# Kernel tuning notes

Measured on AMD Instinct MI355X. Metric: run time of the kernel, lower is better.

Reference implementation:

```python
import jax, jax.numpy as jnp
import numpy as np
from jax import lax

B, T, F = 64, 1536, 512
POOL = 6
UNITS = 256
NUM_CLASSES = 250


def _hard_sigmoid(x):
    # Keras hard_sigmoid: clip(0.2*x + 0.5, 0, 1)
    return jnp.clip(0.2 * x + 0.5, 0.0, 1.0)


def setup_inputs() -> dict:
    key = jax.random.key(0)
    ks = jax.random.split(key, 6)
    x = jax.random.normal(ks[0], (B, T, F), dtype=jnp.float32)
    # ConvLSTM1D with kernel_size=1 over a length-1 spatial axis == dense gates.
    W = jax.random.normal(ks[1], (F, 4 * UNITS), dtype=jnp.float32) * 0.05   # input kernel
    R = jax.random.normal(ks[2], (UNITS, 4 * UNITS), dtype=jnp.float32) * 0.05  # recurrent kernel
    b = jnp.zeros((4 * UNITS,), dtype=jnp.float32)
    Wd = jax.random.normal(ks[3], (UNITS, NUM_CLASSES), dtype=jnp.float32) * 0.05
    bd = jnp.zeros((NUM_CLASSES,), dtype=jnp.float32)
    return {"x": x, "W": W, "R": R, "b": b, "Wd": Wd, "bd": bd}


def reference(x, W, R, b, Wd, bd):
    Bx, Tx, Fx = x.shape
    Tp = Tx // POOL
    # AveragePooling1D(pool_size=6) over time
    xp = x[:, : Tp * POOL].reshape(Bx, Tp, POOL, Fx).mean(axis=2)  # [B, Tp, F]
    # Precompute input-to-gate contribution for all steps (one big GEMM)
    zx = jnp.einsum('btf,fg->btg', xp, W) + b  # [B, Tp, 4U]
    z_seq = jnp.swapaxes(zx, 0, 1)  # [Tp, B, 4U]

    h0 = jnp.zeros((Bx, UNITS), dtype=x.dtype)
    c0 = jnp.zeros((Bx, UNITS), dtype=x.dtype)

    def step(carry, z_t):
        h, c = carry
        z = z_t + h @ R  # [B, 4U]
        i, f, g, o = jnp.split(z, 4, axis=-1)  # Keras gate order: i, f, c, o
        i = _hard_sigmoid(i)
        f = _hard_sigmoid(f)
        g = jnp.tanh(g)
        o = _hard_sigmoid(o)
        c = f * c + i * g
        h = o * jnp.tanh(c)
        return (h, c), None

    (h, _), _ = lax.scan(step, (h0, c0), z_seq)
    # squeeze(-2) + dropout(eval: identity) + flatten -> [B, UNITS]
    logits = h @ Wd + bd
    return jax.nn.softmax(logits, axis=-1)
```

## Files before the change

### kernel.cpp

```cpp
#include <hip/hip_runtime.h>
#include <hip/hip_bf16.h>

#define BB 64
#define TT 1536
#define FF 512
#define TP 256
#define UU 256
#define GG 1024
#define NC 250

typedef _Float16 h2_t __attribute__((ext_vector_type(2)));
typedef _Float16 f16x8 __attribute__((ext_vector_type(8)));
typedef float f32x4 __attribute__((ext_vector_type(4)));

#if defined(__has_builtin)
#  if __has_builtin(__builtin_amdgcn_fdot2)
#    define FDOT2(a, b, c) __builtin_amdgcn_fdot2((a), (b), (c), false)
#  endif
#endif
#ifndef FDOT2
__device__ __forceinline__ float fdot2_fb(h2_t a, h2_t b, float c) {
    return c + (float)a[0] * (float)b[0] + (float)a[1] * (float)b[1];
}
#  define FDOT2(a, b, c) fdot2_fb((a), (b), (c))
#endif

#define BC(u) __builtin_bit_cast(h2_t, (u))

__device__ __forceinline__ float hsig(float z) {
    return fminf(fmaxf(fmaf(z, 0.2f, 0.5f), 0.0f), 1.0f);
}

__device__ __forceinline__ float ftanh(float x) {
    float ax = fabsf(x);
    float e = __expf(-2.0f * ax);
    float t = (1.0f - e) / (1.0f + e);
    return copysignf(t, x);
}

__device__ __forceinline__ void dot4(float& z, const uint4& r, const uint4& h) {
    z = FDOT2(BC(r.x), BC(h.x), z);
    z = FDOT2(BC(r.y), BC(h.y), z);
    z = FDOT2(BC(r.z), BC(h.z), z);
    z = FDOT2(BC(r.w), BC(h.w), z);
}

#if defined(__has_builtin) && __has_builtin(__builtin_amdgcn_mov_dpp)
template <int CTRL>
__device__ __forceinline__ float qperm(float v) {
    return __builtin_bit_cast(float,
        __builtin_amdgcn_mov_dpp(__builtin_bit_cast(int, v), CTRL, 0xf, 0xf, true));
}
#else
template <int CTRL>
__device__ __forceinline__ float qperm(float v) {
    return __shfl_xor(v, CTRL == 0xB1 ? 1 : 2, 64);
}
#endif

__global__ __launch_bounds__(256) void pool_kernel(const float* __restrict__ x,
                                                   _Float16* __restrict__ xph) {
    int idx = blockIdx.x * 256 + threadIdx.x;
    int f4 = (idx & 127) << 2;
    int m = idx >> 7;
    int tp = m & (TP - 1);
    int b = m >> 8;
    const float* src = x + ((size_t)b * TT + (size_t)tp * 6) * FF + f4;
    float sx = 0.f, sy = 0.f, sz = 0.f, sw = 0.f;
#pragma unroll
    for (int j = 0; j < 6; ++j) {
        float4 v = *(const float4*)&src[j * FF];
        sx += v.x; sy += v.y; sz += v.z; sw += v.w;
    }
    const float r6 = 1.0f / 6.0f;
    h2_t lo, hi;
    lo[0] = (_Float16)(sx * r6); lo[1] = (_Float16)(sy * r6);
    hi[0] = (_Float16)(sz * r6); hi[1] = (_Float16)(sw * r6);
    float2 w = make_float2(__builtin_bit_cast(float, lo), __builtin_bit_cast(float, hi));
    *(float2*)&xph[(size_t)m * FF + f4] = w;
}

template <int PERM>
__global__ __launch_bounds__(256) void transpose_cvt(const float* __restrict__ in,
                                                     _Float16* __restrict__ out,
                                                     int K, int N) {
    __shared__ _Float16 tile[32][42];
    const int r = threadIdx.x >> 3;
    const int c4 = (threadIdx.x & 7) << 2;
    const int n0 = blockIdx.x << 5;
    const int k0 = blockIdx.y << 5;
    float4 v = *(const float4*)&in[(size_t)(k0 + r) * N + n0 + c4];
    tile[r][c4 + 0] = (_Float16)v.x;
    tile[r][c4 + 1] = (_Float16)v.y;
    tile[r][c4 + 2] = (_Float16)v.z;
    tile[r][c4 + 3] = (_Float16)v.w;
    __syncthreads();
    int n = n0 + r;
    int orow = PERM ? (((n & 255) << 2) | (n >> 8)) : n;
    h2_t lo, hi;
    lo[0] = tile[c4 + 0][r]; lo[1] = tile[c4 + 1][r];
    hi[0] = tile[c4 + 2][r]; hi[1] = tile[c4 + 3][r];
    float2 w = make_float2(__builtin_bit_cast(float, lo), __builtin_bit_cast(float, hi));
    *(float2*)&out[(size_t)orow * K + k0 + c4] = w;
}

__global__ __launch_bounds__(256, 2) void gemm_zx_mfma(const _Float16* __restrict__ Ah,
                                                       const _Float16* __restrict__ Bt,
                                                       const float* __restrict__ bias,
                                                       float* __restrict__ C) {
    __shared__ _Float16 As[128 * 40];
    __shared__ _Float16 Bs[128 * 40];
    const int tid = threadIdx.x;
    const int bn = blockIdx.x * 128;
    const int bm = blockIdx.y * 128;
    const int wave = tid >> 6, lane = tid & 63;
    const int wm = (wave & 1) * 64, wn = (wave >> 1) * 64;
    const int l15 = lane & 15, q8 = (lane >> 4) * 8;
    const int srow = tid >> 1, shalf = tid & 1;

    f32x4 acc[4][4] = {};
    const uint4* ag = (const uint4*)(Ah + (size_t)(bm + srow) * FF);
    const uint4* bg = (const uint4*)(Bt + (size_t)(bn + srow) * FF);
    uint4* as_st = (uint4*)As + 5 * srow + 2 * shalf;
    uint4* bs_st = (uint4*)Bs + 5 * srow + 2 * shalf;

    for (int k0 = 0; k0 < FF; k0 += 32) {
        int qi = (k0 >> 3) + shalf * 2;
        uint4 a0 = ag[qi], a1 = ag[qi + 1];
        uint4 b0 = bg[qi], b1 = bg[qi + 1];
        __syncthreads();
        as_st[0] = a0; as_st[1] = a1;
        bs_st[0] = b0; bs_st[1] = b1;
        __syncthreads();
        f16x8 af[4], bf[4];
#pragma unroll
        for (int mt = 0; mt < 4; ++mt)
            af[mt] = *(const f16x8*)&As[(wm + 16 * mt + l15) * 40 + q8];
#pragma unroll
        for (int nt = 0; nt < 4; ++nt)
            bf[nt] = *(const f16x8*)&Bs[(wn + 16 * nt + l15) * 40 + q8];
#pragma unroll
        for (int mt = 0; mt < 4; ++mt)
#pragma unroll
            for (int nt = 0; nt < 4; ++nt)
                acc[mt][nt] = __builtin_amdgcn_mfma_f32_16x16x32_f16(af[mt], bf[nt],
                                                                    acc[mt][nt], 0, 0, 0);
    }
    const int rq = (lane >> 4) * 4;
#pragma unroll
    for (int nt = 0; nt < 4; ++nt) {
        int col = bn + wn + 16 * nt + l15;
        int oc = ((col & 3) << 8) | (col >> 2);
        float bv = bias[oc];
#pragma unroll
        for (int mt = 0; mt < 4; ++mt) {
#pragma unroll
            for (int r = 0; r < 4; ++r) {
                int row = bm + wm + 16 * mt + rq + r;
                C[(size_t)row * GG + col] = ((const float*)&acc[mt][nt])[r] + bv;
            }
        }
    }
}

__global__ __launch_bounds__(512, 1) void lstm_scan(const float* __restrict__ zx,
                                                    const _Float16* __restrict__ Rt,
                                                    float* __restrict__ hfin) {
    __shared__ uint4 Rl[14][512];
    __shared__ __align__(16) _Float16 hbuf[2][2][136];
    const int b = blockIdx.x;
    const int t = threadIdx.x;
    const int u = t >> 1, s = t & 1;

    const uint4* rt = (const uint4*)Rt + (size_t)u * 32 + (s << 4);

    uint4 rv[46];
#pragma unroll
    for (int g = 0; g < 4; ++g) {
        const int RC = (g < 2) ? 12 : 11;
        const int RO = (g == 0) ? 0 : (g == 1) ? 12 : (g == 2) ? 24 : 35;
        const int LO = (g == 0) ? 0 : (g == 1) ? 3 : (g == 2) ? 6 : 10;
#pragma unroll
        for (int kk = 0; kk < 15; ++kk) {
            if (kk < RC) rv[RO + kk] = rt[g * 8192 + kk];
            else         Rl[LO + kk - RC][t] = rt[g * 8192 + kk];
        }
    }
    if (t < 272) ((unsigned*)hbuf)[t] = 0u;
    float c = 0.0f;
    const float4* zxp = (const float4*)zx + (size_t)b * TP * UU + u;
    float4 zn = zxp[0];
    __syncthreads();

#pragma unroll 1
    for (int step = 0; step < TP; ++step) {
        float4 zn2 = zxp[(size_t)((step + 1 < TP) ? step + 1 : step) * UU];
        uint4 st[4];
#pragma unroll
        for (int g = 0; g < 4; ++g) st[g] = rt[g * 8192 + 15];

        const uint4* hq = (const uint4*)hbuf[step & 1][s];
        float z[4] = {0.f, 0.f, 0.f, 0.f};
#pragma unroll
        for (int kk = 0; kk < 16; ++kk) {
            uint4 hh = hq[kk];
#pragma unroll
            for (int g = 0; g < 4; ++g) {
                const int RC = (g < 2) ? 12 : 11;
                const int RO = (g == 0) ? 0 : (g == 1) ? 12 : (g == 2) ? 24 : 35;
                const int LO = (g == 0) ? 0 : (g == 1) ? 3 : (g == 2) ? 6 : 10;
                if (kk < RC)      dot4(z[g], rv[RO + kk], hh);
                else if (kk < 15) dot4(z[g], Rl[LO + kk - RC][t], hh);
                else              dot4(z[g], st[g], hh);
            }
        }
#pragma unroll
        for (int g = 0; g < 4; ++g) z[g] += qperm<0xB1>(z[g]);

        float ig = hsig(z[0] + zn.x);
        float fg = hsig(z[1] + zn.y);
        float gv = ftanh(z[2] + zn.z);
        float og = hsig(z[3] + zn.w);
        c = fmaf(fg, c, ig * gv);
        float h = og * ftanh(c);
        if (s == 0) {
            hbuf[(step + 1) & 1][u >> 7][u & 127] = (_Float16)h;
            if (step == TP - 1) hfin[(size_t)b * UU + u] = h;
        }
        zn = zn2;
        __syncthreads();
    }
}

__global__ __launch_bounds__(256) void dense_softmax(const float* __restrict__ hfin,
                                                     const float* __restrict__ Wd,
                                                     const float* __restrict__ bd,
                                                     float* __restrict__ out) {
    __shared__ __align__(16) float hbuf[UU];
    __shared__ float red[256];
    const int b = blockIdx.x;
    const int tid = threadIdx.x;
    hbuf[tid] = hfin[(size_t)b * UU + tid];
    __syncthreads();
    float logit = -3.0e38f;
    if (tid < NC) {
        float acc = bd[tid];
        for (int u = 0; u < UU; u += 4) {
            float4 hv = *(const float4*)&hbuf[u];
            acc = fmaf(hv.x, Wd[(size_t)(u + 0) * NC + tid], acc);
            acc = fmaf(hv.y, Wd[(size_t)(u + 1) * NC + tid], acc);
            acc = fmaf(hv.z, Wd[(size_t)(u + 2) * NC + tid], acc);
            acc = fmaf(hv.w, Wd[(size_t)(u + 3) * NC + tid], acc);
        }
        logit = acc;
    }
    red[tid] = logit;
    __syncthreads();
    for (int sdx = 128; sdx > 0; sdx >>= 1) {
        if (tid < sdx) red[tid] = fmaxf(red[tid], red[tid + sdx]);
        __syncthreads();
    }
    float mx = red[0];
    __syncthreads();
    float e = (tid < NC) ? expf(logit - mx) : 0.0f;
    red[tid] = e;
    __syncthreads();
    for (int sdx = 128; sdx > 0; sdx >>= 1) {
        if (tid < sdx) red[tid] += red[tid + sdx];
        __syncthreads();
    }
    if (tid < NC) out[(size_t)b * NC + tid] = e / red[0];
}

extern "C" void kernel_launch(void* const* d_in, const int* in_sizes, int n_in,
                              void* d_out, int out_size, void* d_ws, size_t ws_size,
                              hipStream_t stream) {
    const float* x  = (const float*)d_in[0];
    const float* W  = (const float*)d_in[1];
    const float* R  = (const float*)d_in[2];
    const float* bv = (const float*)d_in[3];
    const float* Wd = (const float*)d_in[4];
    const float* bd = (const float*)d_in[5];
    float* out = (float*)d_out;

    char* ws = (char*)d_ws;
    _Float16* xph = (_Float16*)ws;
    float* zx = (float*)(ws + 16777216);
    _Float16* Wtp = (_Float16*)(ws + 83886080);
    _Float16* Rt  = (_Float16*)(ws + 84934656);
    float* hfin = (float*)(ws + 85458944);

    hipLaunchKernelGGL(pool_kernel, dim3(8192), dim3(256), 0, stream, x, xph);
    hipLaunchKernelGGL(HIP_KERNEL_NAME(transpose_cvt<1>), dim3(32, 16), dim3(256), 0,
                       stream, W, Wtp, FF, GG);
    hipLaunchKernelGGL(HIP_KERNEL_NAME(transpose_cvt<0>), dim3(32, 8), dim3(256), 0,
                       stream, R, Rt, UU, GG);
    hipLaunchKernelGGL(gemm_zx_mfma, dim3(8, 128), dim3(256), 0, stream,
                       xph, Wtp, bv, zx);
    hipLaunchKernelGGL(lstm_scan, dim3(64), dim3(512), 0, stream, zx, Rt, hfin);
    hipLaunchKernelGGL(dense_softmax, dim3(64), dim3(256), 0, stream, hfin, Wd, bd, out);
}
```

Before: 697.9 us.

## Stream half of recurrent weights from L2 with prefetch, relayout R for coalescing

The scan kernel no longer keeps most of R in registers plus LDS. It holds only the even k-chunks in registers (32 uint4) and streams the odd chunks from a newly relaid-out global buffer Rq through a rotating prefetch ring of 8 entries inside the step loop. A new conv_rq kernel builds a coalesced per-thread layout of R, and Rt is moved into the zx region, which is safe because it is consumed before the GEMM writes there. The register footprint drops so the kernel can target two waves per EU. The cost is L2 traffic for half of R on every timestep of the serial recurrence.

```diff
diff --git a/kernel.cpp b/kernel.cpp
--- a/kernel.cpp
+++ b/kernel.cpp
@@ -57,6 +57,8 @@
     return __shfl_xor(v, CTRL == 0xB1 ? 1 : 2, 64);
 }
 #endif
+
+#define PIN4(q) asm volatile("" : "+v"((q).x), "+v"((q).y), "+v"((q).z), "+v"((q).w))
 
 __global__ __launch_bounds__(256) void pool_kernel(const float* __restrict__ x,
                                                    _Float16* __restrict__ xph) {
@@ -104,6 +106,17 @@
     *(float2*)&out[(size_t)orow * K + k0 + c4] = w;
 }
 
+__global__ __launch_bounds__(256) void conv_rq(const _Float16* __restrict__ Rt,
+                                               uint4* __restrict__ Rq) {
+    int d = blockIdx.x * 256 + threadIdx.x;
+    int q = d >> 9, t = d & 511;
+    int g = q >> 4, kk = q & 15;
+    int u = t >> 1, s = t & 1;
+    int c = (g << 8) | u;
+    int k0 = (s << 7) | (kk << 3);
+    Rq[d] = *(const uint4*)&Rt[(size_t)c * 256 + k0];
+}
+
 __global__ __launch_bounds__(256, 2) void gemm_zx_mfma(const _Float16* __restrict__ Ah,
                                                        const _Float16* __restrict__ Bt,
                                                        const float* __restrict__ bias,
@@ -163,29 +176,36 @@
     }
 }
 
-__global__ __launch_bounds__(512, 1) void lstm_scan(const float* __restrict__ zx,
-                                                    const _Float16* __restrict__ Rt,
-                                                    float* __restrict__ hfin) {
-    __shared__ uint4 Rl[14][512];
+__global__ __launch_bounds__(512)
+__attribute__((amdgpu_waves_per_eu(2)))
+void lstm_scan(const float* __restrict__ zx,
+               const uint4* __restrict__ Rq,
+               float* __restrict__ hfin) {
     __shared__ __align__(16) _Float16 hbuf[2][2][136];
     const int b = blockIdx.x;
     const int t = threadIdx.x;
     const int u = t >> 1, s = t & 1;
 
-    const uint4* rt = (const uint4*)Rt + (size_t)u * 32 + (s << 4);
-
-    uint4 rv[46];
-#pragma unroll
-    for (int g = 0; g < 4; ++g) {
-        const int RC = (g < 2) ? 12 : 11;
-        const int RO = (g == 0) ? 0 : (g == 1) ? 12 : (g == 2) ? 24 : 35;
-        const int LO = (g == 0) ? 0 : (g == 1) ? 3 : (g == 2) ? 6 : 10;
-#pragma unroll
-        for (int kk = 0; kk < 15; ++kk) {
-            if (kk < RC) rv[RO + kk] = rt[g * 8192 + kk];
-            else         Rl[LO + kk - RC][t] = rt[g * 8192 + kk];
-        }
-    }
+    const uint4* rqt = Rq + t;
+
+    uint4 rv[4][8];
+#pragma unroll
+    for (int g = 0; g < 4; ++g)
+#pragma unroll
+        for (int e = 0; e < 8; ++e)
+            rv[g][e] = rqt[(size_t)(g * 16 + 2 * e) * 512];
+#pragma unroll
+    for (int g = 0; g < 4; ++g)
+#pragma unroll
+        for (int e = 0; e < 8; ++e)
+            PIN4(rv[g][e]);
+
+    uint4 stb[8][4];
+#pragma unroll
+    for (int g = 0; g < 4; ++g) stb[0][g] = rqt[(size_t)(g * 16 + 1) * 512];
+#pragma unroll
+    for (int g = 0; g < 4; ++g) stb[1][g] = rqt[(size_t)(g * 16 + 3) * 512];
+
     if (t < 272) ((unsigned*)hbuf)[t] = 0u;
     float c = 0.0f;
     const float4* zxp = (const float4*)zx + (size_t)b * TP * UU + u;
@@ -195,23 +215,23 @@
 #pragma unroll 1
     for (int step = 0; step < TP; ++step) {
         float4 zn2 = zxp[(size_t)((step + 1 < TP) ? step + 1 : step) * UU];
-        uint4 st[4];
-#pragma unroll
-        for (int g = 0; g < 4; ++g) st[g] = rt[g * 8192 + 15];
-
         const uint4* hq = (const uint4*)hbuf[step & 1][s];
         float z[4] = {0.f, 0.f, 0.f, 0.f};
 #pragma unroll
         for (int kk = 0; kk < 16; ++kk) {
+            if ((kk & 1) == 0) {
+                const int tgt = (kk + 5) & 15;
+#pragma unroll
+                for (int g = 0; g < 4; ++g)
+                    stb[tgt >> 1][g] = rqt[(size_t)(g * 16 + tgt) * 512];
+            }
             uint4 hh = hq[kk];
-#pragma unroll
-            for (int g = 0; g < 4; ++g) {
-                const int RC = (g < 2) ? 12 : 11;
-                const int RO = (g == 0) ? 0 : (g == 1) ? 12 : (g == 2) ? 24 : 35;
-                const int LO = (g == 0) ? 0 : (g == 1) ? 3 : (g == 2) ? 6 : 10;
-                if (kk < RC)      dot4(z[g], rv[RO + kk], hh);
-                else if (kk < 15) dot4(z[g], Rl[LO + kk - RC][t], hh);
-                else              dot4(z[g], st[g], hh);
+            if (kk & 1) {
+#pragma unroll
+                for (int g = 0; g < 4; ++g) dot4(z[g], stb[kk >> 1][g], hh);
+            } else {
+#pragma unroll
+                for (int g = 0; g < 4; ++g) dot4(z[g], rv[g][kk >> 1], hh);
             }
         }
 #pragma unroll
@@ -286,8 +306,9 @@
     char* ws = (char*)d_ws;
     _Float16* xph = (_Float16*)ws;
     float* zx = (float*)(ws + 16777216);
+    _Float16* Rt = (_Float16*)(ws + 16777216);
     _Float16* Wtp = (_Float16*)(ws + 83886080);
-    _Float16* Rt  = (_Float16*)(ws + 84934656);
+    uint4* Rq = (uint4*)(ws + 84934656);
     float* hfin = (float*)(ws + 85458944);
 
     hipLaunchKernelGGL(pool_kernel, dim3(8192), dim3(256), 0, stream, x, xph);
@@ -295,8 +316,9 @@
                        stream, W, Wtp, FF, GG);
     hipLaunchKernelGGL(HIP_KERNEL_NAME(transpose_cvt<0>), dim3(32, 8), dim3(256), 0,
                        stream, R, Rt, UU, GG);
+    hipLaunchKernelGGL(conv_rq, dim3(128), dim3(256), 0, stream, Rt, Rq);
     hipLaunchKernelGGL(gemm_zx_mfma, dim3(8, 128), dim3(256), 0, stream,
                        xph, Wtp, bv, zx);
-    hipLaunchKernelGGL(lstm_scan, dim3(64), dim3(512), 0, stream, zx, Rt, hfin);
+    hipLaunchKernelGGL(lstm_scan, dim3(64), dim3(512), 0, stream, zx, Rq, hfin);
     hipLaunchKernelGGL(dense_softmax, dim3(64), dim3(256), 0, stream, hfin, Wd, bd, out);
 }
```

New measurement: 1.927 ms. +176.2%, slower.

## Split LSTM recurrence across four threads per unit with pre-swizzled weights

Applied to the files above, without the earlier changes.

The scan kernel now runs 1024 threads per batch row, with four threads sharing each hidden unit's dot product instead of two. The per-step global reload of the last R slice goes away: a new conv_rq kernel reorders R into a thread-major layout, and the scan keeps it entirely in registers plus shared memory. This halves the per-thread work on the serial critical path but adds an extra cross-lane reduction step and a larger block barrier each step. Rt is now staged in the zx buffer region before the GEMM overwrites it.

```diff
diff --git a/kernel.cpp b/kernel.cpp
--- a/kernel.cpp
+++ b/kernel.cpp
@@ -104,6 +104,17 @@
     *(float2*)&out[(size_t)orow * K + k0 + c4] = w;
 }
 
+__global__ __launch_bounds__(256) void conv_rq(const _Float16* __restrict__ Rt,
+                                               uint4* __restrict__ Rq) {
+    int d = blockIdx.x * 256 + threadIdx.x;
+    int q = d >> 10, t = d & 1023;
+    int g = q >> 3, kk = q & 7;
+    int u = t >> 2, s = t & 3;
+    int col = (g << 8) | u;
+    int k0 = (s << 6) | (kk << 3);
+    Rq[d] = *(const uint4*)&Rt[(size_t)col * 256 + k0];
+}
+
 __global__ __launch_bounds__(256, 2) void gemm_zx_mfma(const _Float16* __restrict__ Ah,
                                                        const _Float16* __restrict__ Bt,
                                                        const float* __restrict__ bias,
@@ -163,30 +174,36 @@
     }
 }
 
-__global__ __launch_bounds__(512, 1) void lstm_scan(const float* __restrict__ zx,
-                                                    const _Float16* __restrict__ Rt,
-                                                    float* __restrict__ hfin) {
-    __shared__ uint4 Rl[14][512];
-    __shared__ __align__(16) _Float16 hbuf[2][2][136];
+__global__ __launch_bounds__(1024) void lstm_scan(const float* __restrict__ zx,
+                                                  const uint4* __restrict__ Rq,
+                                                  float* __restrict__ hfin) {
+    __shared__ uint4 Rl[9][1024];
+    __shared__ __align__(16) _Float16 hbuf[2][4][72];
     const int b = blockIdx.x;
     const int t = threadIdx.x;
-    const int u = t >> 1, s = t & 1;
-
-    const uint4* rt = (const uint4*)Rt + (size_t)u * 32 + (s << 4);
-
-    uint4 rv[46];
-#pragma unroll
-    for (int g = 0; g < 4; ++g) {
-        const int RC = (g < 2) ? 12 : 11;
-        const int RO = (g == 0) ? 0 : (g == 1) ? 12 : (g == 2) ? 24 : 35;
-        const int LO = (g == 0) ? 0 : (g == 1) ? 3 : (g == 2) ? 6 : 10;
-#pragma unroll
-        for (int kk = 0; kk < 15; ++kk) {
-            if (kk < RC) rv[RO + kk] = rt[g * 8192 + kk];
-            else         Rl[LO + kk - RC][t] = rt[g * 8192 + kk];
-        }
-    }
-    if (t < 272) ((unsigned*)hbuf)[t] = 0u;
+    const int u = t >> 2, s = t & 3;
+
+    const uint4* rqt = Rq + t;
+
+    uint4 rv0[6], rv1[6], rv2[6], rv3[5];
+#pragma unroll
+    for (int kk = 0; kk < 6; ++kk) {
+        rv0[kk] = rqt[(0 * 8 + kk) * 1024];
+        rv1[kk] = rqt[(1 * 8 + kk) * 1024];
+        rv2[kk] = rqt[(2 * 8 + kk) * 1024];
+        if (kk < 5) rv3[kk] = rqt[(3 * 8 + kk) * 1024];
+    }
+    Rl[0][t] = rqt[(0 * 8 + 6) * 1024];
+    Rl[1][t] = rqt[(0 * 8 + 7) * 1024];
+    Rl[2][t] = rqt[(1 * 8 + 6) * 1024];
+    Rl[3][t] = rqt[(1 * 8 + 7) * 1024];
+    Rl[4][t] = rqt[(2 * 8 + 6) * 1024];
+    Rl[5][t] = rqt[(2 * 8 + 7) * 1024];
+    Rl[6][t] = rqt[(3 * 8 + 5) * 1024];
+    Rl[7][t] = rqt[(3 * 8 + 6) * 1024];
+    Rl[8][t] = rqt[(3 * 8 + 7) * 1024];
+
+    if (t < 288) ((unsigned*)hbuf)[t] = 0u;
     float c = 0.0f;
     const float4* zxp = (const float4*)zx + (size_t)b * TP * UU + u;
     float4 zn = zxp[0];
@@ -195,36 +212,29 @@
 #pragma unroll 1
     for (int step = 0; step < TP; ++step) {
         float4 zn2 = zxp[(size_t)((step + 1 < TP) ? step + 1 : step) * UU];
-        uint4 st[4];
-#pragma unroll
-        for (int g = 0; g < 4; ++g) st[g] = rt[g * 8192 + 15];
-
-        const uint4* hq = (const uint4*)hbuf[step & 1][s];
-        float z[4] = {0.f, 0.f, 0.f, 0.f};
-#pragma unroll
-        for (int kk = 0; kk < 16; ++kk) {
-            uint4 hh = hq[kk];
-#pragma unroll
-            for (int g = 0; g < 4; ++g) {
-                const int RC = (g < 2) ? 12 : 11;
-                const int RO = (g == 0) ? 0 : (g == 1) ? 12 : (g == 2) ? 24 : 35;
-                const int LO = (g == 0) ? 0 : (g == 1) ? 3 : (g == 2) ? 6 : 10;
-                if (kk < RC)      dot4(z[g], rv[RO + kk], hh);
-                else if (kk < 15) dot4(z[g], Rl[LO + kk - RC][t], hh);
-                else              dot4(z[g], st[g], hh);
-            }
+        const char* hbase = (const char*)hbuf[step & 1] + s * 144;
+        float z0 = 0.f, z1 = 0.f, z2 = 0.f, z3 = 0.f;
+#pragma unroll
+        for (int kk = 0; kk < 8; ++kk) {
+            uint4 hh = *(const uint4*)(hbase + kk * 16);
+            if (kk < 6) dot4(z0, rv0[kk], hh); else dot4(z0, Rl[kk - 6][t], hh);
+            if (kk < 6) dot4(z1, rv1[kk], hh); else dot4(z1, Rl[2 + kk - 6][t], hh);
+            if (kk < 6) dot4(z2, rv2[kk], hh); else dot4(z2, Rl[4 + kk - 6][t], hh);
+            if (kk < 5) dot4(z3, rv3[kk], hh); else dot4(z3, Rl[6 + kk - 5][t], hh);
         }
-#pragma unroll
-        for (int g = 0; g < 4; ++g) z[g] += qperm<0xB1>(z[g]);
-
-        float ig = hsig(z[0] + zn.x);
-        float fg = hsig(z[1] + zn.y);
-        float gv = ftanh(z[2] + zn.z);
-        float og = hsig(z[3] + zn.w);
+        z0 += qperm<0xB1>(z0); z0 += qperm<0x4E>(z0);
+        z1 += qperm<0xB1>(z1); z1 += qperm<0x4E>(z1);
+        z2 += qperm<0xB1>(z2); z2 += qperm<0x4E>(z2);
+        z3 += qperm<0xB1>(z3); z3 += qperm<0x4E>(z3);
+
+        float ig = hsig(z0 + zn.x);
+        float fg = hsig(z1 + zn.y);
+        float gv = ftanh(z2 + zn.z);
+        float og = hsig(z3 + zn.w);
         c = fmaf(fg, c, ig * gv);
         float h = og * ftanh(c);
         if (s == 0) {
-            hbuf[(step + 1) & 1][u >> 7][u & 127] = (_Float16)h;
+            hbuf[(step + 1) & 1][u >> 6][u & 63] = (_Float16)h;
             if (step == TP - 1) hfin[(size_t)b * UU + u] = h;
         }
         zn = zn2;
@@ -286,8 +296,9 @@
     char* ws = (char*)d_ws;
     _Float16* xph = (_Float16*)ws;
     float* zx = (float*)(ws + 16777216);
+    _Float16* Rt = (_Float16*)(ws + 16777216);
     _Float16* Wtp = (_Float16*)(ws + 83886080);
-    _Float16* Rt  = (_Float16*)(ws + 84934656);
+    uint4* Rq = (uint4*)(ws + 84934656);
     float* hfin = (float*)(ws + 85458944);
 
     hipLaunchKernelGGL(pool_kernel, dim3(8192), dim3(256), 0, stream, x, xph);
@@ -295,8 +306,9 @@
                        stream, W, Wtp, FF, GG);
     hipLaunchKernelGGL(HIP_KERNEL_NAME(transpose_cvt<0>), dim3(32, 8), dim3(256), 0,
                        stream, R, Rt, UU, GG);
+    hipLaunchKernelGGL(conv_rq, dim3(128), dim3(256), 0, stream, Rt, Rq);
     hipLaunchKernelGGL(gemm_zx_mfma, dim3(8, 128), dim3(256), 0, stream,
                        xph, Wtp, bv, zx);
-    hipLaunchKernelGGL(lstm_scan, dim3(64), dim3(512), 0, stream, zx, Rt, hfin);
+    hipLaunchKernelGGL(lstm_scan, dim3(64), dim3(1024), 0, stream, zx, Rq, hfin);
     hipLaunchKernelGGL(dense_softmax, dim3(64), dim3(256), 0, stream, hfin, Wd, bd, out);
 }
```

Measured after the change: 805.8 us. 1.15x slower.
